# Kernel optimization log

Hardware: AMD Instinct MI355X
Metric: run time of the kernel (lower is better)

Reference implementation:

```python
import jax, jax.numpy as jnp
import numpy as np

B, S, HID = 1, 2048, 4096
NH, NKV, HD = 32, 8, 128
GROUPS = NH // NKV
SCALING = HD ** -0.5


def approx_matmul(a, b):
    # BaselineApproxMatmulFP16: matmul performed in fp16 precision
    return jnp.matmul(a.astype(jnp.float16), b.astype(jnp.float16)).astype(a.dtype)


def rotate_half(x):
    x1, x2 = jnp.split(x, 2, axis=-1)
    return jnp.concatenate([-x2, x1], axis=-1)


def setup_inputs() -> dict:
    key = jax.random.key(0)
    ks = jax.random.split(key, 6)
    hidden_states = jax.random.normal(ks[0], (B, S, HID), jnp.float32)
    # Proper RoPE tables (HF llama convention: freqs duplicated across halves)
    inv_freq = 1.0 / (10000.0 ** (jnp.arange(0, HD, 2, dtype=jnp.float32) / HD))
    t = jnp.arange(S, dtype=jnp.float32)
    freqs = jnp.outer(t, inv_freq)                      # [S, HD/2]
    emb = jnp.concatenate([freqs, freqs], axis=-1)      # [S, HD]
    cos = jnp.cos(emb)[None]                            # [B, S, HD]
    sin = jnp.sin(emb)[None]
    # Additive causal mask [B,1,S,S]
    causal = jnp.triu(jnp.full((S, S), -1e9, jnp.float32), k=1)[None, None]
    scale = 0.02
    wq = jax.random.normal(ks[1], (HID, NH * HD), jnp.float32) * scale
    wk = jax.random.normal(ks[2], (HID, NKV * HD), jnp.float32) * scale
    wv = jax.random.normal(ks[3], (HID, NKV * HD), jnp.float32) * scale
    wo = jax.random.normal(ks[4], (NH * HD, HID), jnp.float32) * scale
    return {"hidden_states": hidden_states, "cos": cos, "sin": sin,
            "attn_mask": causal, "wq": wq, "wk": wk, "wv": wv, "wo": wo}


def reference(hidden_states, cos, sin, attn_mask, wq, wk, wv, wo):
    x = hidden_states
    # projections -> [B, heads, S, HD]
    q = (x @ wq).reshape(B, S, NH, HD).transpose(0, 2, 1, 3)
    k = (x @ wk).reshape(B, S, NKV, HD).transpose(0, 2, 1, 3)
    v = (x @ wv).reshape(B, S, NKV, HD).transpose(0, 2, 1, 3)
    # RoPE
    c = cos[:, None]  # [B,1,S,HD]
    s = sin[:, None]
    q = q * c + rotate_half(q) * s
    k = k * c + rotate_half(k) * s
    # repeat_kv (GQA): [B,NKV,S,HD] -> [B,NH,S,HD]
    k = jnp.repeat(k, GROUPS, axis=1)
    v = jnp.repeat(v, GROUPS, axis=1)
    # eager attention with fp16 approx matmul
    attn = approx_matmul(q, k.transpose(0, 1, 3, 2)) * SCALING  # [B,NH,S,S]
    attn = attn + attn_mask
    attn = jax.nn.softmax(attn.astype(jnp.float32), axis=-1).astype(q.dtype)
    out = approx_matmul(attn, v)                                # [B,NH,S,HD]
    out = out.transpose(0, 2, 1, 3).reshape(B, S, NH * HD)
    return out @ wo
```

## Files before the change

kernel.cpp:

```cpp
#include <hip/hip_runtime.h>
#include <hip/hip_bf16.h>
#include <hip/hip_fp16.h>

typedef _Float16 half8 __attribute__((ext_vector_type(8)));
typedef _Float16 half4 __attribute__((ext_vector_type(4)));
typedef float f32x4 __attribute__((ext_vector_type(4)));
typedef unsigned int u32;

#define S_LEN 2048
#define HID_DIM 4096
#define N_HEADS 32
#define N_KV 8
#define HEAD_DIM 128
#define SCALE_QK 0.08838834764831845f

__device__ __forceinline__ void async16(void* lds, const void* gptr) {
  __builtin_amdgcn_global_load_lds(
      (const __attribute__((address_space(1))) u32*)gptr,
      (__attribute__((address_space(3))) u32*)lds, 16, 0, 0);
}

__global__ void conv_f32_f16(const float* __restrict__ src, _Float16* __restrict__ dst, int n4) {
  int i = blockIdx.x * 256 + threadIdx.x;
  if (i < n4) {
    float4 v = ((const float4*)src)[i];
    half4 h;
    h[0] = (_Float16)v.x; h[1] = (_Float16)v.y; h[2] = (_Float16)v.z; h[3] = (_Float16)v.w;
    ((half4*)dst)[i] = h;
  }
}

__global__ void transpose_f32_f16(const float* __restrict__ src, _Float16* __restrict__ dst,
                                  int R, int C) {
  __shared__ _Float16 tile[64][33];
  int bx = blockIdx.x;
  int by = blockIdx.y;
  int x = threadIdx.x, y = threadIdx.y;
#pragma unroll
  for (int k = 0; k < 8; k++)
    tile[y + 8 * k][x] = (_Float16)src[(long)(by * 64 + y + 8 * k) * C + bx * 32 + x];
  __syncthreads();
  int tid = y * 32 + x;
  int r = tid & 63;
  int cb = tid >> 6;
#pragma unroll
  for (int w = 0; w < 8; w++) {
    int c = w * 4 + cb;
    dst[(long)(bx * 32 + c) * R + by * 64 + r] = tile[r][c];
  }
}

template <int NHEADS>
__global__ void rope_tiled(_Float16* __restrict__ t, const float* __restrict__ cosb,
                           const float* __restrict__ sinb) {
  int idx = blockIdx.x * 256 + threadIdx.x;
  int slo = idx & 15;
  int d8 = (idx >> 4) & 7;
  int h = (idx >> 7) % NHEADS;
  int s16 = idx / (128 * NHEADS);
  int s = s16 * 16 + slo;
  int d0 = d8 * 8;
  long c0 = (long)(h * 128 + s16) * 4;
  long base = (c0 + (d0 >> 5)) * 512 + ((d0 >> 3) & 3) * 128 + slo * 8;
  half8 a = *(half8*)(t + base);
  half8 b = *(half8*)(t + base + 1024);
  const float* cp = cosb + s * 128 + d0;
  const float* sp = sinb + s * 128 + d0;
  half8 olo, ohi;
#pragma unroll
  for (int j = 0; j < 8; j++) {
    float c = cp[j], sn = sp[j];
    float av = (float)a[j], bv = (float)b[j];
    olo[j] = (_Float16)(av * c - bv * sn);
    ohi[j] = (_Float16)(bv * c + av * sn);
  }
  *(half8*)(t + base) = olo;
  *(half8*)(t + base + 1024) = ohi;
}

__global__ __launch_bounds__(256, 3) void gemm_qkv(
    const _Float16* __restrict__ A, const _Float16* __restrict__ BtQ,
    const _Float16* __restrict__ BtKV, _Float16* __restrict__ Qt,
    _Float16* __restrict__ Kt, _Float16* __restrict__ Vt) {
  __shared__ _Float16 As[128 * 64];
  __shared__ _Float16 Bs[128 * 64];
  const int K = 4096;
  const int tid = threadIdx.x, lane = tid & 63, wid = tid >> 6;
  const int row0 = blockIdx.y * 128;
  const int col0 = blockIdx.x * 128;
  const int wm = wid >> 1, wn = wid & 1;
  const int lr = lane & 15, lg = lane >> 4;

  const _Float16* bbase = (col0 < 4096) ? (BtQ + (long)col0 * K)
                                        : (BtKV + (long)(col0 - 4096) * K);
  const int scol = ((lane & 7) ^ ((lane >> 3) & 7)) * 8;
  const _Float16* aptr = A + (long)(row0 + wid * 32 + (lane >> 3)) * K + scol;
  const _Float16* bptr = bbase + (long)(wid * 32 + (lane >> 3)) * K + scol;
  _Float16* alds = As + (wid * 4) * 512;
  _Float16* blds = Bs + (wid * 4) * 512;

  f32x4 acc[4][4] = {};
  for (int k0 = 0; k0 < K; k0 += 64) {
#pragma unroll
    for (int j = 0; j < 4; j++) {
      async16(alds + j * 512, aptr + k0 + (long)j * 8 * K);
      async16(blds + j * 512, bptr + k0 + (long)j * 8 * K);
    }
    __syncthreads();
    half8 a[2][4], b[2][4];
#pragma unroll
    for (int kk = 0; kk < 2; kk++)
#pragma unroll
      for (int mf = 0; mf < 4; mf++) {
        a[kk][mf] = *(const half8*)&As[(wm * 64 + mf * 16 + lr) * 64 +
                                       (((kk * 4 + lg) ^ (lr & 7)) * 8)];
        b[kk][mf] = *(const half8*)&Bs[(wn * 64 + mf * 16 + lr) * 64 +
                                       (((kk * 4 + lg) ^ (lr & 7)) * 8)];
      }
#pragma unroll
    for (int kk = 0; kk < 2; kk++)
#pragma unroll
      for (int mf = 0; mf < 4; mf++)
#pragma unroll
        for (int nf = 0; nf < 4; nf++)
          acc[mf][nf] =
              __builtin_amdgcn_mfma_f32_16x16x32_f16(a[kk][mf], b[kk][nf], acc[mf][nf], 0, 0, 0);
    __syncthreads();
  }

#pragma unroll
  for (int mf = 0; mf < 4; mf++) {
#pragma unroll
    for (int nf = 0; nf < 4; nf++) {
      int rbase = row0 + wm * 64 + mf * 16 + lg * 4;
      int col = col0 + wn * 64 + nf * 16 + lr;
      if (col0 < 4096) {
        int h = col >> 7, d = col & 127;
        long off = ((long)((h * 128 + (rbase >> 4)) * 4 + (d >> 5))) * 512 +
                   ((d >> 3) & 3) * 128 + (rbase & 15) * 8 + (d & 7);
#pragma unroll
        for (int i = 0; i < 4; i++) Qt[off + i * 8] = (_Float16)acc[mf][nf][i];
      } else if (col0 < 5120) {
        int gc = col - 4096;
        int g = gc >> 7, d = gc & 127;
        long off = ((long)((g * 128 + (rbase >> 4)) * 4 + (d >> 5))) * 512 +
                   ((d >> 3) & 3) * 128 + (rbase & 15) * 8 + (d & 7);
#pragma unroll
        for (int i = 0; i < 4; i++) Kt[off + i * 8] = (_Float16)acc[mf][nf][i];
      } else {
        int gc = col - 5120;
        int gq = gc >> 7, d = gc & 127;
        int dt = d >> 4, lrr = d & 15;
        int kvb = rbase >> 5, lgv = (rbase >> 3) & 3, j = rbase & 7;
        half4 v;
#pragma unroll
        for (int i = 0; i < 4; i++) v[i] = (_Float16)acc[mf][nf][i];
        long off = ((long)(gq * 64 + kvb) * 8 + dt) * 512 + (lgv * 16 + lrr) * 8 + j;
        *(half4*)&Vt[off] = v;
      }
    }
  }
}

__global__ __launch_bounds__(256, 3) void gemm_out(
    const _Float16* __restrict__ A, const _Float16* __restrict__ Bt,
    float* __restrict__ C) {
  __shared__ _Float16 As[128 * 64];
  __shared__ _Float16 Bs[128 * 64];
  const int K = 4096;
  const int tid = threadIdx.x, lane = tid & 63, wid = tid >> 6;
  const int row0 = blockIdx.y * 128;
  const int col0 = blockIdx.x * 128;
  const int wm = wid >> 1, wn = wid & 1;
  const int lr = lane & 15, lg = lane >> 4;

  const int scol = ((lane & 7) ^ ((lane >> 3) & 7)) * 8;
  const _Float16* aptr = A + (long)(row0 + wid * 32 + (lane >> 3)) * K + scol;
  const _Float16* bptr = Bt + (long)(col0 + wid * 32 + (lane >> 3)) * K + scol;
  _Float16* alds = As + (wid * 4) * 512;
  _Float16* blds = Bs + (wid * 4) * 512;

  f32x4 acc[4][4] = {};
  for (int k0 = 0; k0 < K; k0 += 64) {
#pragma unroll
    for (int j = 0; j < 4; j++) {
      async16(alds + j * 512, aptr + k0 + (long)j * 8 * K);
      async16(blds + j * 512, bptr + k0 + (long)j * 8 * K);
    }
    __syncthreads();
    half8 a[2][4], b[2][4];
#pragma unroll
    for (int kk = 0; kk < 2; kk++)
#pragma unroll
      for (int mf = 0; mf < 4; mf++) {
        a[kk][mf] = *(const half8*)&As[(wm * 64 + mf * 16 + lr) * 64 +
                                       (((kk * 4 + lg) ^ (lr & 7)) * 8)];
        b[kk][mf] = *(const half8*)&Bs[(wn * 64 + mf * 16 + lr) * 64 +
                                       (((kk * 4 + lg) ^ (lr & 7)) * 8)];
      }
#pragma unroll
    for (int kk = 0; kk < 2; kk++)
#pragma unroll
      for (int mf = 0; mf < 4; mf++)
#pragma unroll
        for (int nf = 0; nf < 4; nf++)
          acc[mf][nf] =
              __builtin_amdgcn_mfma_f32_16x16x32_f16(a[kk][mf], b[kk][nf], acc[mf][nf], 0, 0, 0);
    __syncthreads();
  }
#pragma unroll
  for (int mf = 0; mf < 4; mf++)
#pragma unroll
    for (int nf = 0; nf < 4; nf++) {
      int rbase = row0 + wm * 64 + mf * 16 + lg * 4;
      int col = col0 + wn * 64 + nf * 16 + lr;
#pragma unroll
      for (int i = 0; i < 4; i++)
        C[(long)(rbase + i) * 4096 + col] = acc[mf][nf][i];
    }
}

__global__ __launch_bounds__(256, 3) void attn_kernel(
    const _Float16* __restrict__ Qt, const _Float16* __restrict__ Kt,
    const _Float16* __restrict__ Vt, _Float16* __restrict__ O) {
  __shared__ _Float16 Klds[2][4096];
  __shared__ _Float16 Vlds[2][4096];
  __shared__ _Float16 P_lds[4][512];
  const int tid = threadIdx.x;
  const int lane = tid & 63;
  const int wid = tid >> 6;
  const int bid = blockIdx.x;
  const int g = bid & 7;
  const int qidx = bid >> 3;
  const int qt16 = (qidx < 64) ? (2 * qidx) : (2 * (127 - qidx) + 1);
  const int h = g * 4 + wid;
  const int qrow0 = qt16 * 16;
  const int ntiles = (qrow0 + 47) >> 5;
  const int lr = lane & 15;
  const int lg = lane >> 4;

  half8 qf[4];
  {
    const _Float16* qp = Qt + ((long)(h * 128 + qt16) * 4) * 512 + lane * 8;
#pragma unroll
    for (int t = 0; t < 4; t++) qf[t] = *(const half8*)(qp + t * 512);
  }

  const _Float16* kgb = Kt + (long)g * 128 * 2048 + lane * 8;
  const _Float16* vgb = Vt + (long)g * 64 * 4096 + lane * 8;

  {
    async16(&Klds[0][(2 * wid) * 512], kgb + (2 * wid) * 512);
    async16(&Klds[0][(2 * wid + 1) * 512], kgb + (2 * wid + 1) * 512);
    async16(&Vlds[0][(2 * wid) * 512], vgb + (2 * wid) * 512);
    async16(&Vlds[0][(2 * wid + 1) * 512], vgb + (2 * wid + 1) * 512);
  }
  __syncthreads();

  f32x4 oacc[8] = {};
  float mrow[4] = {-1e30f, -1e30f, -1e30f, -1e30f};
  float lsum[4] = {0.f, 0.f, 0.f, 0.f};

  for (int t = 0; t < ntiles; t++) {
    const int kb = t * 32;
    const int cur = t & 1;
    if (t + 1 < ntiles) {
      const _Float16* ks = kgb + (long)(t + 1) * 4096;
      const _Float16* vs = vgb + (long)(t + 1) * 4096;
      async16(&Klds[cur ^ 1][(2 * wid) * 512], ks + (2 * wid) * 512);
      async16(&Klds[cur ^ 1][(2 * wid + 1) * 512], ks + (2 * wid + 1) * 512);
      async16(&Vlds[cur ^ 1][(2 * wid) * 512], vs + (2 * wid) * 512);
      async16(&Vlds[cur ^ 1][(2 * wid + 1) * 512], vs + (2 * wid + 1) * 512);
    }

    half8 kf[8];
#pragma unroll
    for (int c = 0; c < 8; c++)
      kf[c] = *(const half8*)&Klds[cur][c * 512 + lane * 8];
    half8 vf[8];
#pragma unroll
    for (int dt = 0; dt < 8; dt++)
      vf[dt] = *(const half8*)&Vlds[cur][dt * 512 + lane * 8];

    f32x4 sacc[2] = {};
#pragma unroll
    for (int s = 0; s < 2; s++)
#pragma unroll
      for (int t2 = 0; t2 < 4; t2++)
        sacc[s] = __builtin_amdgcn_mfma_f32_16x16x32_f16(qf[t2], kf[s * 4 + t2], sacc[s], 0, 0, 0);

    float mx[4];
    bool grow = false;
#pragma unroll
    for (int i = 0; i < 4; i++) {
      int qrow = qrow0 + lg * 4 + i;
      float s0 = sacc[0][i] * SCALE_QK;
      float s1 = sacc[1][i] * SCALE_QK;
      if (kb + lr > qrow) s0 = -1e30f;
      if (kb + 16 + lr > qrow) s1 = -1e30f;
      sacc[0][i] = s0; sacc[1][i] = s1;
      mx[i] = fmaxf(s0, s1);
      grow |= (mx[i] > mrow[i] + 4.0f);
    }
    if (__any((int)grow)) {
#pragma unroll
      for (int i = 0; i < 4; i++) {
        float m = mx[i];
        m = fmaxf(m, __shfl_xor(m, 1));
        m = fmaxf(m, __shfl_xor(m, 2));
        m = fmaxf(m, __shfl_xor(m, 4));
        m = fmaxf(m, __shfl_xor(m, 8));
        float mn = fmaxf(mrow[i], m);
        float scl = __expf(mrow[i] - mn);
        mrow[i] = mn;
        lsum[i] *= scl;
#pragma unroll
        for (int dt = 0; dt < 8; dt++) oacc[dt][i] *= scl;
      }
    }
    float p[2][4];
#pragma unroll
    for (int i = 0; i < 4; i++) {
      p[0][i] = __expf(sacc[0][i] - mrow[i]);
      p[1][i] = __expf(sacc[1][i] - mrow[i]);
      lsum[i] += p[0][i] + p[1][i];
    }

#pragma unroll
    for (int sub = 0; sub < 2; sub++)
#pragma unroll
      for (int i = 0; i < 4; i++)
        P_lds[wid][(lg * 4 + i) * 32 + sub * 16 + lr] = (_Float16)p[sub][i];
    half8 pa = *(const half8*)&P_lds[wid][lr * 32 + lg * 8];

#pragma unroll
    for (int dt = 0; dt < 8; dt++)
      oacc[dt] = __builtin_amdgcn_mfma_f32_16x16x32_f16(pa, vf[dt], oacc[dt], 0, 0, 0);

    __syncthreads();
  }

#pragma unroll
  for (int i = 0; i < 4; i++) {
    float t2 = lsum[i];
    t2 += __shfl_xor(t2, 1);
    t2 += __shfl_xor(t2, 2);
    t2 += __shfl_xor(t2, 4);
    t2 += __shfl_xor(t2, 8);
    lsum[i] = t2;
  }
#pragma unroll
  for (int dt = 0; dt < 8; dt++) {
#pragma unroll
    for (int i = 0; i < 4; i++) {
      float o = oacc[dt][i] / lsum[i];
      O[(long)(qrow0 + lg * 4 + i) * HID_DIM + h * HEAD_DIM + dt * 16 + lr] = (_Float16)o;
    }
  }
}

extern "C" void kernel_launch(void* const* d_in, const int* in_sizes, int n_in,
                              void* d_out, int out_size, void* d_ws, size_t ws_size,
                              hipStream_t stream) {
  const float* x    = (const float*)d_in[0];
  const float* cosb = (const float*)d_in[1];
  const float* sinb = (const float*)d_in[2];
  const float* wq = (const float*)d_in[4];
  const float* wk = (const float*)d_in[5];
  const float* wv = (const float*)d_in[6];
  const float* wo = (const float*)d_in[7];
  float* out = (float*)d_out;

  char* ws = (char*)d_ws;
  _Float16* Xh    = (_Float16*)(ws);
  _Float16* Oattn = Xh;
  _Float16* Qt    = (_Float16*)(ws + (size_t)(16 << 20));
  _Float16* Kt    = (_Float16*)(ws + (size_t)(32 << 20));
  _Float16* Vt    = (_Float16*)(ws + (size_t)(36 << 20));
  _Float16* WqT   = (_Float16*)(ws + (size_t)(40 << 20));
  _Float16* WoT   = WqT;
  _Float16* WkvT  = (_Float16*)d_out;

  dim3 b256(256);
  dim3 tb(32, 8);

  conv_f32_f16<<<dim3(S_LEN * HID_DIM / 4 / 256), b256, 0, stream>>>(x, Xh, S_LEN * HID_DIM / 4);

  transpose_f32_f16<<<dim3(4096 / 32, 4096 / 64), tb, 0, stream>>>(wq, WqT, 4096, 4096);
  transpose_f32_f16<<<dim3(1024 / 32, 4096 / 64), tb, 0, stream>>>(wk, WkvT, 4096, 1024);
  transpose_f32_f16<<<dim3(1024 / 32, 4096 / 64), tb, 0, stream>>>(wv, WkvT + (size_t)1024 * 4096, 4096, 1024);

  gemm_qkv<<<dim3(6144 / 128, S_LEN / 128), b256, 0, stream>>>(Xh, WqT, WkvT, Qt, Kt, Vt);

  rope_tiled<N_HEADS><<<dim3(N_HEADS * 16384 / 256), b256, 0, stream>>>(Qt, cosb, sinb);
  rope_tiled<N_KV><<<dim3(N_KV * 16384 / 256), b256, 0, stream>>>(Kt, cosb, sinb);

  attn_kernel<<<dim3(1024), b256, 0, stream>>>(Qt, Kt, Vt, Oattn);

  transpose_f32_f16<<<dim3(4096 / 32, 4096 / 64), tb, 0, stream>>>(wo, WoT, 4096, 4096);
  gemm_out<<<dim3(4096 / 128, S_LEN / 128), b256, 0, stream>>>(Oattn, WoT, out);
}
```

Baseline: 327.7 us.

## Process two 16-row query groups per wave and fuse Q RoPE into attention

Each attention wave now handles 32 query rows (two 16-row groups) instead of 16, so every K/V tile loaded into LDS and registers feeds twice the MFMA work, and the grid shrinks from 1024 to 512 blocks. The separate RoPE pass over Q is removed and applied in registers when Q fragments are loaded, saving one full read/write of Q. In exchange register pressure roughly doubles (occupancy hint lowered from 3 to 2 blocks per CU), the causal tile count is coarser, and there are fewer blocks to balance across CUs.

```diff
diff --git a/kernel.cpp b/kernel.cpp
--- a/kernel.cpp
+++ b/kernel.cpp
@@ -220,30 +220,45 @@
     }
 }
 
-__global__ __launch_bounds__(256, 3) void attn_kernel(
+__global__ __launch_bounds__(256, 2) void attn_kernel(
     const _Float16* __restrict__ Qt, const _Float16* __restrict__ Kt,
-    const _Float16* __restrict__ Vt, _Float16* __restrict__ O) {
+    const _Float16* __restrict__ Vt, _Float16* __restrict__ O,
+    const float* __restrict__ cosb, const float* __restrict__ sinb) {
   __shared__ _Float16 Klds[2][4096];
   __shared__ _Float16 Vlds[2][4096];
-  __shared__ _Float16 P_lds[4][512];
+  __shared__ _Float16 P_lds[4][1024];
   const int tid = threadIdx.x;
   const int lane = tid & 63;
   const int wid = tid >> 6;
   const int bid = blockIdx.x;
   const int g = bid & 7;
   const int qidx = bid >> 3;
-  const int qt16 = (qidx < 64) ? (2 * qidx) : (2 * (127 - qidx) + 1);
+  const int qt32 = (qidx < 32) ? (2 * qidx) : (2 * (63 - qidx) + 1);
   const int h = g * 4 + wid;
-  const int qrow0 = qt16 * 16;
-  const int ntiles = (qrow0 + 47) >> 5;
+  const int qrow0 = qt32 * 32;
+  const int ntiles = qt32 + 1;
   const int lr = lane & 15;
   const int lg = lane >> 4;
 
-  half8 qf[4];
-  {
-    const _Float16* qp = Qt + ((long)(h * 128 + qt16) * 4) * 512 + lane * 8;
-#pragma unroll
-    for (int t = 0; t < 4; t++) qf[t] = *(const half8*)(qp + t * 512);
+  half8 qf[2][4];
+#pragma unroll
+  for (int rg = 0; rg < 2; rg++) {
+    const _Float16* qp = Qt + ((long)(h * 128 + qt32 * 2 + rg) * 4) * 512 + lane * 8;
+#pragma unroll
+    for (int t = 0; t < 4; t++) qf[rg][t] = *(const half8*)(qp + t * 512);
+    int s = qrow0 + rg * 16 + lr;
+#pragma unroll
+    for (int t = 0; t < 2; t++) {
+      const float* cp = cosb + s * 128 + t * 32 + lg * 8;
+      const float* sp = sinb + s * 128 + t * 32 + lg * 8;
+#pragma unroll
+      for (int j = 0; j < 8; j++) {
+        float c = cp[j], sn = sp[j];
+        float lo = (float)qf[rg][t][j], hi = (float)qf[rg][t + 2][j];
+        qf[rg][t][j]     = (_Float16)(lo * c - hi * sn);
+        qf[rg][t + 2][j] = (_Float16)(hi * c + lo * sn);
+      }
+    }
   }
 
   const _Float16* kgb = Kt + (long)g * 128 * 2048 + lane * 8;
@@ -257,9 +272,9 @@
   }
   __syncthreads();
 
-  f32x4 oacc[8] = {};
-  float mrow[4] = {-1e30f, -1e30f, -1e30f, -1e30f};
-  float lsum[4] = {0.f, 0.f, 0.f, 0.f};
+  f32x4 oacc[2][8] = {};
+  float mrow[2][4] = {{-1e30f, -1e30f, -1e30f, -1e30f}, {-1e30f, -1e30f, -1e30f, -1e30f}};
+  float lsum[2][4] = {};
 
   for (int t = 0; t < ntiles; t++) {
     const int kb = t * 32;
@@ -277,84 +292,101 @@
 #pragma unroll
     for (int c = 0; c < 8; c++)
       kf[c] = *(const half8*)&Klds[cur][c * 512 + lane * 8];
+
+    f32x4 sacc[2][2] = {};
+#pragma unroll
+    for (int s = 0; s < 2; s++)
+#pragma unroll
+      for (int rg = 0; rg < 2; rg++)
+#pragma unroll
+        for (int t2 = 0; t2 < 4; t2++)
+          sacc[s][rg] =
+              __builtin_amdgcn_mfma_f32_16x16x32_f16(qf[rg][t2], kf[s * 4 + t2], sacc[s][rg], 0, 0, 0);
+
     half8 vf[8];
 #pragma unroll
     for (int dt = 0; dt < 8; dt++)
       vf[dt] = *(const half8*)&Vlds[cur][dt * 512 + lane * 8];
 
-    f32x4 sacc[2] = {};
-#pragma unroll
-    for (int s = 0; s < 2; s++)
-#pragma unroll
-      for (int t2 = 0; t2 < 4; t2++)
-        sacc[s] = __builtin_amdgcn_mfma_f32_16x16x32_f16(qf[t2], kf[s * 4 + t2], sacc[s], 0, 0, 0);
-
-    float mx[4];
+    float mx[2][4];
     bool grow = false;
 #pragma unroll
+    for (int rg = 0; rg < 2; rg++)
+#pragma unroll
+      for (int i = 0; i < 4; i++) {
+        int qrow = qrow0 + rg * 16 + lg * 4 + i;
+        float s0 = sacc[0][rg][i] * SCALE_QK;
+        float s1 = sacc[1][rg][i] * SCALE_QK;
+        if (kb + lr > qrow) s0 = -1e30f;
+        if (kb + 16 + lr > qrow) s1 = -1e30f;
+        sacc[0][rg][i] = s0; sacc[1][rg][i] = s1;
+        mx[rg][i] = fmaxf(s0, s1);
+        grow |= (mx[rg][i] > mrow[rg][i] + 4.0f);
+      }
+    if (__any((int)grow)) {
+#pragma unroll
+      for (int rg = 0; rg < 2; rg++)
+#pragma unroll
+        for (int i = 0; i < 4; i++) {
+          float m = mx[rg][i];
+          m = fmaxf(m, __shfl_xor(m, 1));
+          m = fmaxf(m, __shfl_xor(m, 2));
+          m = fmaxf(m, __shfl_xor(m, 4));
+          m = fmaxf(m, __shfl_xor(m, 8));
+          float mn = fmaxf(mrow[rg][i], m);
+          float scl = __expf(mrow[rg][i] - mn);
+          mrow[rg][i] = mn;
+          lsum[rg][i] *= scl;
+#pragma unroll
+          for (int dt = 0; dt < 8; dt++) oacc[rg][dt][i] *= scl;
+        }
+    }
+#pragma unroll
+    for (int rg = 0; rg < 2; rg++) {
+      float p0[4], p1[4];
+#pragma unroll
+      for (int i = 0; i < 4; i++) {
+        p0[i] = __expf(sacc[0][rg][i] - mrow[rg][i]);
+        p1[i] = __expf(sacc[1][rg][i] - mrow[rg][i]);
+        lsum[rg][i] += p0[i] + p1[i];
+      }
+#pragma unroll
+      for (int i = 0; i < 4; i++) {
+        P_lds[wid][rg * 512 + (lg * 4 + i) * 32 + lr] = (_Float16)p0[i];
+        P_lds[wid][rg * 512 + (lg * 4 + i) * 32 + 16 + lr] = (_Float16)p1[i];
+      }
+    }
+    half8 pa0 = *(const half8*)&P_lds[wid][lr * 32 + lg * 8];
+    half8 pa1 = *(const half8*)&P_lds[wid][512 + lr * 32 + lg * 8];
+
+#pragma unroll
+    for (int dt = 0; dt < 8; dt++) {
+      oacc[0][dt] = __builtin_amdgcn_mfma_f32_16x16x32_f16(pa0, vf[dt], oacc[0][dt], 0, 0, 0);
+      oacc[1][dt] = __builtin_amdgcn_mfma_f32_16x16x32_f16(pa1, vf[dt], oacc[1][dt], 0, 0, 0);
+    }
+
+    __syncthreads();
+  }
+
+#pragma unroll
+  for (int rg = 0; rg < 2; rg++) {
+#pragma unroll
     for (int i = 0; i < 4; i++) {
-      int qrow = qrow0 + lg * 4 + i;
-      float s0 = sacc[0][i] * SCALE_QK;
-      float s1 = sacc[1][i] * SCALE_QK;
-      if (kb + lr > qrow) s0 = -1e30f;
-      if (kb + 16 + lr > qrow) s1 = -1e30f;
-      sacc[0][i] = s0; sacc[1][i] = s1;
-      mx[i] = fmaxf(s0, s1);
-      grow |= (mx[i] > mrow[i] + 4.0f);
-    }
-    if (__any((int)grow)) {
+      float t2 = lsum[rg][i];
+      t2 += __shfl_xor(t2, 1);
+      t2 += __shfl_xor(t2, 2);
+      t2 += __shfl_xor(t2, 4);
+      t2 += __shfl_xor(t2, 8);
+      lsum[rg][i] = t2;
+    }
+#pragma unroll
+    for (int dt = 0; dt < 8; dt++) {
 #pragma unroll
       for (int i = 0; i < 4; i++) {
-        float m = mx[i];
-        m = fmaxf(m, __shfl_xor(m, 1));
-        m = fmaxf(m, __shfl_xor(m, 2));
-        m = fmaxf(m, __shfl_xor(m, 4));
-        m = fmaxf(m, __shfl_xor(m, 8));
-        float mn = fmaxf(mrow[i], m);
-        float scl = __expf(mrow[i] - mn);
-        mrow[i] = mn;
-        lsum[i] *= scl;
-#pragma unroll
-        for (int dt = 0; dt < 8; dt++) oacc[dt][i] *= scl;
-      }
-    }
-    float p[2][4];
-#pragma unroll
-    for (int i = 0; i < 4; i++) {
-      p[0][i] = __expf(sacc[0][i] - mrow[i]);
-      p[1][i] = __expf(sacc[1][i] - mrow[i]);
-      lsum[i] += p[0][i] + p[1][i];
-    }
-
-#pragma unroll
-    for (int sub = 0; sub < 2; sub++)
-#pragma unroll
-      for (int i = 0; i < 4; i++)
-        P_lds[wid][(lg * 4 + i) * 32 + sub * 16 + lr] = (_Float16)p[sub][i];
-    half8 pa = *(const half8*)&P_lds[wid][lr * 32 + lg * 8];
-
-#pragma unroll
-    for (int dt = 0; dt < 8; dt++)
-      oacc[dt] = __builtin_amdgcn_mfma_f32_16x16x32_f16(pa, vf[dt], oacc[dt], 0, 0, 0);
-
-    __syncthreads();
-  }
-
-#pragma unroll
-  for (int i = 0; i < 4; i++) {
-    float t2 = lsum[i];
-    t2 += __shfl_xor(t2, 1);
-    t2 += __shfl_xor(t2, 2);
-    t2 += __shfl_xor(t2, 4);
-    t2 += __shfl_xor(t2, 8);
-    lsum[i] = t2;
-  }
-#pragma unroll
-  for (int dt = 0; dt < 8; dt++) {
-#pragma unroll
-    for (int i = 0; i < 4; i++) {
-      float o = oacc[dt][i] / lsum[i];
-      O[(long)(qrow0 + lg * 4 + i) * HID_DIM + h * HEAD_DIM + dt * 16 + lr] = (_Float16)o;
+        float o = oacc[rg][dt][i] / lsum[rg][i];
+        O[(long)(qrow0 + rg * 16 + lg * 4 + i) * HID_DIM + h * HEAD_DIM + dt * 16 + lr] =
+            (_Float16)o;
+      }
     }
   }
 }
@@ -392,10 +424,9 @@
 
   gemm_qkv<<<dim3(6144 / 128, S_LEN / 128), b256, 0, stream>>>(Xh, WqT, WkvT, Qt, Kt, Vt);
 
-  rope_tiled<N_HEADS><<<dim3(N_HEADS * 16384 / 256), b256, 0, stream>>>(Qt, cosb, sinb);
   rope_tiled<N_KV><<<dim3(N_KV * 16384 / 256), b256, 0, stream>>>(Kt, cosb, sinb);
 
-  attn_kernel<<<dim3(1024), b256, 0, stream>>>(Qt, Kt, Vt, Oattn);
+  attn_kernel<<<dim3(512), b256, 0, stream>>>(Qt, Kt, Vt, Oattn, cosb, sinb);
 
   transpose_f32_f16<<<dim3(4096 / 32, 4096 / 64), tb, 0, stream>>>(wo, WoT, 4096, 4096);
   gemm_out<<<dim3(4096 / 128, S_LEN / 128), b256, 0, stream>>>(Oattn, WoT, out);
```

New measurement: 338.0 us. 3.1% more time.
